# Kernel tuning notes

Hardware: AMD Instinct MI355X
Metric: run time of the kernel (lower is better)

## Reference

```python
import jax, jax.numpy as jnp
import numpy as np

L = 5          # num_layer
D = 300        # emb_dim
N = 100000     # nodes
E = 250000     # edges
G = 4000       # graphs
EPS = 1e-5


def setup_inputs() -> dict:
    key = jax.random.key(0)
    ks = jax.random.split(key, 32)
    f = lambda k, shape, s=0.02: (jax.random.normal(k, shape, dtype=jnp.float32) * s)
    inp = {
        "x_atom": jax.random.randint(ks[0], (N,), 0, 120),
        "x_chir": jax.random.randint(ks[1], (N,), 0, 3),
        "src": jax.random.randint(ks[2], (E,), 0, N),
        "dst": jax.random.randint(ks[3], (E,), 0, N),
        "edge_type": jax.random.randint(ks[4], (E,), 0, 6),
        "edge_dir": jax.random.randint(ks[5], (E,), 0, 3),
        "batch": jnp.sort(jax.random.randint(ks[6], (N,), 0, G)),
        # node feature embeddings
        "x_emb1": f(ks[7], (120, D), 0.1),
        "x_emb2": f(ks[8], (3, D), 0.1),
        # per-layer GIN params (stacked over L)
        "edge_e1": f(ks[9], (L, 6, D), 0.1),
        "edge_e2": f(ks[10], (L, 3, D), 0.1),
        "mlp_w1": f(ks[11], (L, D, 2 * D)),
        "mlp_b1": jnp.zeros((L, 2 * D), jnp.float32),
        "mlp_w2": f(ks[12], (L, 2 * D, D)),
        "mlp_b2": jnp.zeros((L, D), jnp.float32),
        # BatchNorm (inference mode: running stats)
        "bn_gamma": jnp.ones((L, D), jnp.float32),
        "bn_beta": jnp.zeros((L, D), jnp.float32),
        "bn_mean": f(ks[13], (L, D), 0.1),
        "bn_var": jax.random.uniform(ks[14], (L, D), jnp.float32, 0.5, 1.5),
        # virtual node (embedding initialized to zero in the original)
        "vn_emb": jnp.zeros((D,), jnp.float32),
        # vn MLPs: Linear -> LayerNorm -> ReLU -> Linear, L-1 of them
        "vn_w1": f(ks[15], (L - 1, D, D)),
        "vn_b1": jnp.zeros((L - 1, D), jnp.float32),
        "vn_ln_g": jnp.ones((L - 1, D), jnp.float32),
        "vn_ln_b": jnp.zeros((L - 1, D), jnp.float32),
        "vn_w2": f(ks[16], (L - 1, D, D)),
        "vn_b2": jnp.zeros((L - 1, D), jnp.float32),
    }
    return inp


def _forward(x_atom, x_chir, src, dst, edge_type, edge_dir, batch,
             x_emb1, x_emb2, edge_e1, edge_e2, mlp_w1, mlp_b1, mlp_w2, mlp_b2,
             bn_gamma, bn_beta, bn_mean, bn_var,
             vn_emb, vn_w1, vn_b1, vn_ln_g, vn_ln_b, vn_w2, vn_b2):
    n = x_atom.shape[0]
    # node counts per graph for mean pooling (guard empty graphs)
    counts = jnp.maximum(
        jax.ops.segment_sum(jnp.ones((n, 1), jnp.float32), batch, num_segments=G), 1.0)

    h = x_emb1[x_atom] + x_emb2[x_chir]                      # [N, D]
    vn_h = jnp.broadcast_to(vn_emb, (G, D))                  # [G, D]
    h = h + vn_h[batch]

    for l in range(L):
        # --- GIN conv: message = h[src] + edge_emb, scatter-add to dst ---
        edge_emb = edge_e1[l][edge_type] + edge_e2[l][edge_dir]   # [E, D]
        msg = h[src] + edge_emb
        aggr = jax.ops.segment_sum(msg, dst, num_segments=n)      # [N, D]
        # self loops: x_j = h[i], self-loop attr = (type 4, dir 0)
        aggr = aggr + h + (edge_e1[l][4] + edge_e2[l][0])
        # MLP: Linear(D,2D) -> ReLU -> Linear(2D,D)
        z = jax.nn.relu(aggr @ mlp_w1[l] + mlp_b1[l]) @ mlp_w2[l] + mlp_b2[l]
        # BatchNorm1d (eval): running stats
        z = (z - bn_mean[l]) * (bn_gamma[l] * jax.lax.rsqrt(bn_var[l] + EPS)) + bn_beta[l]
        if l < L - 1:
            z = jax.nn.relu(z)  # (dropout is identity at inference)
            # --- virtual node update ---
            pooled = jax.ops.segment_sum(z, batch, num_segments=G) / counts
            vn_new = pooled + vn_h                                # [G, D]
            t = vn_new @ vn_w1[l] + vn_b1[l]
            mu = jnp.mean(t, axis=-1, keepdims=True)
            var = jnp.var(t, axis=-1, keepdims=True)
            t = (t - mu) * jax.lax.rsqrt(var + EPS) * vn_ln_g[l] + vn_ln_b[l]
            vn_h = jax.nn.relu(t) @ vn_w2[l] + vn_b2[l]
            z = z + vn_h[batch]
        h = z
    return h


def reference(x_atom, x_chir, src, dst, edge_type, edge_dir, batch,
              x_emb1, x_emb2, edge_e1, edge_e2, mlp_w1, mlp_b1, mlp_w2, mlp_b2,
              bn_gamma, bn_beta, bn_mean, bn_var,
              vn_emb, vn_w1, vn_b1, vn_ln_g, vn_ln_b, vn_w2, vn_b2):
    return _forward(x_atom, x_chir, src, dst, edge_type, edge_dir, batch,
                    x_emb1, x_emb2, edge_e1, edge_e2, mlp_w1, mlp_b1, mlp_w2, mlp_b2,
                    bn_gamma, bn_beta, bn_mean, bn_var,
                    vn_emb, vn_w1, vn_b1, vn_ln_g, vn_ln_b, vn_w2, vn_b2)
```

## Files before the change

kernel.cpp:

```cpp
#include <hip/hip_runtime.h>

#define DD   300
#define DD2  600
#define GG   4000
#define LL   5
#define BN_EPS 1e-5f

typedef float f32x4  __attribute__((ext_vector_type(4)));
typedef short bf16x8 __attribute__((ext_vector_type(8)));

__device__ __forceinline__ unsigned short f2bf(float f) {
    unsigned int x = __float_as_uint(f);
    unsigned int r = (x + 0x7FFFu + ((x >> 16) & 1u)) >> 16;
    return (unsigned short)r;
}

__global__ __launch_bounds__(256) void k_hist(const int* __restrict__ idx, int* __restrict__ cnt, int n) {
    int i = blockIdx.x * 256 + threadIdx.x;
    if (i < n) atomicAdd(&cnt[idx[i]], 1);
}

__global__ __launch_bounds__(256) void k_scan1(const int* __restrict__ in, int* __restrict__ bsum, int n) {
    int t = threadIdx.x;
    int i = blockIdx.x * 256 + t;
    int v = (i < n) ? in[i] : 0;
    for (int off = 32; off >= 1; off >>= 1) v += __shfl_down(v, off, 64);
    __shared__ int s[4];
    if ((t & 63) == 0) s[t >> 6] = v;
    __syncthreads();
    if (t == 0) bsum[blockIdx.x] = s[0] + s[1] + s[2] + s[3];
}
__global__ __launch_bounds__(1024) void k_scan2(int* __restrict__ bsum, int nb) {
    __shared__ int s[1024];
    int t = threadIdx.x;
    int v = (t < nb) ? bsum[t] : 0;
    s[t] = v;
    __syncthreads();
    for (int off = 1; off < 1024; off <<= 1) {
        int u = (t >= off) ? s[t - off] : 0;
        __syncthreads();
        s[t] += u;
        __syncthreads();
    }
    if (t < nb) bsum[t] = s[t] - v;
}
__global__ __launch_bounds__(256) void k_scan3(const int* __restrict__ in, const int* __restrict__ boff,
                                               int* __restrict__ out, int n, int total) {
    __shared__ int s[256];
    int t = threadIdx.x;
    int i = blockIdx.x * 256 + t;
    int v = (i < n) ? in[i] : 0;
    s[t] = v;
    __syncthreads();
    for (int off = 1; off < 256; off <<= 1) {
        int u = (t >= off) ? s[t - off] : 0;
        __syncthreads();
        s[t] += u;
        __syncthreads();
    }
    if (i < n) out[i] = boff[blockIdx.x] + s[t] - v;
    if (i == 0) out[n] = total;
}

__global__ __launch_bounds__(256) void k_place(const int* __restrict__ src, const int* __restrict__ dst,
                                               const int* __restrict__ ety, const int* __restrict__ edir,
                                               const int* __restrict__ rowptr, int* __restrict__ cursor,
                                               int* __restrict__ einfo, int E) {
    int e = blockIdx.x * 256 + threadIdx.x;
    if (e >= E) return;
    int d = dst[e];
    int pos = rowptr[d] + atomicAdd(&cursor[d], 1);
    einfo[pos] = src[e] | ((ety[e] * 3 + edir[e]) << 20);
}

__global__ __launch_bounds__(256) void k_comb(const float* __restrict__ e1, const float* __restrict__ e2,
                                              float* __restrict__ comb) {
    int c = blockIdx.x, l = blockIdx.y;
    const float* r1 = e1 + ((size_t)l * 6 + (c / 3)) * DD;
    const float* r2 = e2 + ((size_t)l * 3 + (c % 3)) * DD;
    float* out = comb + ((size_t)l * 18 + c) * DD;
    for (int d = threadIdx.x; d < DD; d += 256) out[d] = r1[d] + r2[d];
}

__global__ __launch_bounds__(256) void k_init_h(const int* __restrict__ xa, const int* __restrict__ xc,
                                                const float* __restrict__ emb1, const float* __restrict__ emb2,
                                                const float* __restrict__ vne,
                                                float* __restrict__ h, int N) {
    int n = blockIdx.x;
    if (n >= N) return;
    int a = xa[n], c = xc[n];
    for (int d = threadIdx.x; d < DD; d += 256)
        h[(size_t)n * DD + d] = emb1[(size_t)a * DD + d] + emb2[(size_t)c * DD + d] + vne[d];
}

__global__ __launch_bounds__(256) void k_init_vn(const float* __restrict__ vne, float* __restrict__ vnh) {
    int g = blockIdx.x;
    for (int d = threadIdx.x; d < DD; d += 256) vnh[(size_t)g * DD + d] = vne[d];
}

__global__ __launch_bounds__(256) void k_aggr(const float* __restrict__ h,
                                              const int* __restrict__ rowptr, const int* __restrict__ einfo,
                                              const float* __restrict__ comb,
                                              const int* __restrict__ batch, const float* __restrict__ vnh,
                                              int use_vn,
                                              unsigned short* __restrict__ aggrb, int N, int Npad) {
    const int node = blockIdx.x * 4 + (threadIdx.x >> 6);
    const int lane = threadIdx.x & 63;
    if (node >= Npad) return;
    unsigned short* out = aggrb + (size_t)node * 320;
    if (node >= N) {
#pragma unroll
        for (int j = 0; j < 5; j++) out[lane + 64 * j] = 0;
        return;
    }
    float acc[5];
    const float* sc = comb + 12 * DD;
    const int p0 = rowptr[node], p1 = rowptr[node + 1];
    if (use_vn) {
        {
            const float* hs = h + (size_t)node * DD;
            const float* vs = vnh + (size_t)batch[node] * DD;
#pragma unroll
            for (int j = 0; j < 5; j++) {
                int d = lane + 64 * j;
                acc[j] = (d < DD) ? hs[d] + sc[d] + vs[d] : 0.f;
            }
        }
        for (int p = p0; p < p1; p++) {
            int info = einfo[p];
            int s = info & 0xFFFFF;
            const float* hr = h + (size_t)s * DD;
            const float* cr = comb + (size_t)(info >> 20) * DD;
            const float* vr = vnh + (size_t)batch[s] * DD;
#pragma unroll
            for (int j = 0; j < 5; j++) {
                int d = lane + 64 * j;
                if (d < DD) acc[j] += hr[d] + cr[d] + vr[d];
            }
        }
    } else {
        {
            const float* hs = h + (size_t)node * DD;
#pragma unroll
            for (int j = 0; j < 5; j++) {
                int d = lane + 64 * j;
                acc[j] = (d < DD) ? hs[d] + sc[d] : 0.f;
            }
        }
        for (int p = p0; p < p1; p++) {
            int info = einfo[p];
            const float* hr = h + (size_t)(info & 0xFFFFF) * DD;
            const float* cr = comb + (size_t)(info >> 20) * DD;
#pragma unroll
            for (int j = 0; j < 5; j++) {
                int d = lane + 64 * j;
                if (d < DD) acc[j] += hr[d] + cr[d];
            }
        }
    }
#pragma unroll
    for (int j = 0; j < 5; j++) {
        int d = lane + 64 * j;
        out[d] = (d < DD) ? f2bf(acc[j]) : (unsigned short)0;
    }
}

__global__ __launch_bounds__(256) void k_convw(const float* __restrict__ w, short* __restrict__ wt,
                                               int K, int Nn, int KP, int NP) {
    int n = blockIdx.x;
    int l = blockIdx.y;
    const float* wl = w + (size_t)l * K * Nn;
    short* wtl = wt + (size_t)l * NP * KP;
    for (int k = threadIdx.x; k < KP; k += 256) {
        float v = (k < K && n < Nn) ? wl[(size_t)k * Nn + n] : 0.f;
        wtl[(size_t)n * KP + k] = (short)f2bf(v);
    }
}

__global__ __launch_bounds__(256) void k_padb(const float* __restrict__ b, float* __restrict__ bp) {
    int l = blockIdx.y;
    int n = blockIdx.x * 256 + threadIdx.x;
    if (n < 640) bp[(size_t)l * 640 + n] = (n < DD2) ? b[(size_t)l * DD2 + n] : 0.f;
}

__global__ __launch_bounds__(256) void k_gemm1(const unsigned short* __restrict__ aggrb,
                                               const short* __restrict__ w1t,
                                               const float* __restrict__ b1p,
                                               unsigned short* __restrict__ hidden) {
    __shared__ short sA[2][64][40];
    __shared__ short sB[2][160][40];
    const int t  = threadIdx.x;
    const int m0 = blockIdx.x * 64;
    const int n0 = blockIdx.y * 160;
    const int ar = t >> 2, aq = (t & 3) << 3;

    {
        *(float4*)&sA[0][ar][aq] = *(const float4*)(aggrb + (size_t)(m0 + ar) * 320 + aq);
#pragma unroll
        for (int i = 0; i < 3; i++) {
            int c = t + (i << 8);
            if (c < 640) {
                int br = c >> 2, bq = (c & 3) << 3;
                *(float4*)&sB[0][br][bq] = *(const float4*)(w1t + (size_t)(n0 + br) * 320 + bq);
            }
        }
    }
    __syncthreads();

    const int lane = t & 63;
    const int w    = t >> 6;
    const int mrow = (w << 4) + (lane & 15);
    const int kb   = (lane >> 4) << 3;
    const int col  = lane & 15;
    const int rq   = (lane >> 4) << 2;

    f32x4 acc[10];
#pragma unroll
    for (int nt = 0; nt < 10; nt++) acc[nt] = (f32x4){0.f, 0.f, 0.f, 0.f};

    for (int ks = 0; ks < 10; ks++) {
        const int nb = ks & 1;
        const bool have = (ks + 1) < 10;
        float4 avr, bv0, bv1, bv2;
        if (have) {
            const int k0 = (ks + 1) << 5;
            avr = *(const float4*)(aggrb + (size_t)(m0 + ar) * 320 + k0 + aq);
            int c = t;
            bv0 = *(const float4*)(w1t + (size_t)(n0 + (c >> 2)) * 320 + k0 + ((c & 3) << 3));
            c = t + 256;
            bv1 = *(const float4*)(w1t + (size_t)(n0 + (c >> 2)) * 320 + k0 + ((c & 3) << 3));
            if (t < 128) {
                c = t + 512;
                bv2 = *(const float4*)(w1t + (size_t)(n0 + (c >> 2)) * 320 + k0 + ((c & 3) << 3));
            }
        }
        bf16x8 a = *(const bf16x8*)&sA[nb][mrow][kb];
#pragma unroll
        for (int nt = 0; nt < 10; nt++) {
            bf16x8 b = *(const bf16x8*)&sB[nb][(nt << 4) + col][kb];
            acc[nt] = __builtin_amdgcn_mfma_f32_16x16x32_bf16(a, b, acc[nt], 0, 0, 0);
        }
        if (have) {
            *(float4*)&sA[nb ^ 1][ar][aq] = avr;
            int c = t;
            *(float4*)&sB[nb ^ 1][c >> 2][(c & 3) << 3] = bv0;
            c = t + 256;
            *(float4*)&sB[nb ^ 1][c >> 2][(c & 3) << 3] = bv1;
            if (t < 128) {
                c = t + 512;
                *(float4*)&sB[nb ^ 1][c >> 2][(c & 3) << 3] = bv2;
            }
        }
        __syncthreads();
    }

#pragma unroll
    for (int nt = 0; nt < 10; nt++) {
        int n = n0 + (nt << 4) + col;
        float bias = b1p[n];
        int mbase = m0 + (w << 4) + rq;
#pragma unroll
        for (int r = 0; r < 4; r++) {
            float vz = fmaxf(acc[nt][r] + bias, 0.f);
            hidden[(size_t)(mbase + r) * 640 + n] = f2bf(vz);
        }
    }
}

__global__ __launch_bounds__(256) void k_gemm2(const unsigned short* __restrict__ hidden,
                                               const short* __restrict__ w2t,
                                               const float* __restrict__ b2,
                                               const float* __restrict__ bng, const float* __restrict__ bnb,
                                               const float* __restrict__ bnm, const float* __restrict__ bnv,
                                               float* __restrict__ h, int N, int relu_out) {
    __shared__ short sA[2][64][40];
    __shared__ short sB[2][160][40];
    const int t  = threadIdx.x;
    const int m0 = blockIdx.x * 64;
    const int n0 = blockIdx.y * 160;
    const int ar = t >> 2, aq = (t & 3) << 3;

    {
        *(float4*)&sA[0][ar][aq] = *(const float4*)(hidden + (size_t)(m0 + ar) * 640 + aq);
#pragma unroll
        for (int i = 0; i < 3; i++) {
            int c = t + (i << 8);
            if (c < 640) {
                int br = c >> 2, bq = (c & 3) << 3;
                *(float4*)&sB[0][br][bq] = *(const float4*)(w2t + (size_t)(n0 + br) * 640 + bq);
            }
        }
    }
    __syncthreads();

    const int lane = t & 63;
    const int w    = t >> 6;
    const int mrow = (w << 4) + (lane & 15);
    const int kb   = (lane >> 4) << 3;
    const int col  = lane & 15;
    const int rq   = (lane >> 4) << 2;

    f32x4 acc[10];
#pragma unroll
    for (int nt = 0; nt < 10; nt++) acc[nt] = (f32x4){0.f, 0.f, 0.f, 0.f};

    for (int ks = 0; ks < 20; ks++) {
        const int nb = ks & 1;
        const bool have = (ks + 1) < 20;
        float4 avr, bv0, bv1, bv2;
        if (have) {
            const int k0 = (ks + 1) << 5;
            avr = *(const float4*)(hidden + (size_t)(m0 + ar) * 640 + k0 + aq);
            int c = t;
            bv0 = *(const float4*)(w2t + (size_t)(n0 + (c >> 2)) * 640 + k0 + ((c & 3) << 3));
            c = t + 256;
            bv1 = *(const float4*)(w2t + (size_t)(n0 + (c >> 2)) * 640 + k0 + ((c & 3) << 3));
            if (t < 128) {
                c = t + 512;
                bv2 = *(const float4*)(w2t + (size_t)(n0 + (c >> 2)) * 640 + k0 + ((c & 3) << 3));
            }
        }
        bf16x8 a = *(const bf16x8*)&sA[nb][mrow][kb];
#pragma unroll
        for (int nt = 0; nt < 10; nt++) {
            bf16x8 b = *(const bf16x8*)&sB[nb][(nt << 4) + col][kb];
            acc[nt] = __builtin_amdgcn_mfma_f32_16x16x32_bf16(a, b, acc[nt], 0, 0, 0);
        }
        if (have) {
            *(float4*)&sA[nb ^ 1][ar][aq] = avr;
            int c = t;
            *(float4*)&sB[nb ^ 1][c >> 2][(c & 3) << 3] = bv0;
            c = t + 256;
            *(float4*)&sB[nb ^ 1][c >> 2][(c & 3) << 3] = bv1;
            if (t < 128) {
                c = t + 512;
                *(float4*)&sB[nb ^ 1][c >> 2][(c & 3) << 3] = bv2;
            }
        }
        __syncthreads();
    }

#pragma unroll
    for (int nt = 0; nt < 10; nt++) {
        int n = n0 + (nt << 4) + col;
        bool nok = (n < DD);
        float bz = 0.f, sc = 1.f, mB = 0.f, bB = 0.f;
        if (nok) {
            bz = b2[n];
            sc = bng[n] * rsqrtf(bnv[n] + BN_EPS);
            mB = bnm[n];
            bB = bnb[n];
        }
        int mbase = m0 + (w << 4) + rq;
#pragma unroll
        for (int r = 0; r < 4; r++) {
            int m = mbase + r;
            if (nok && m < N) {
                float z = (acc[nt][r] + bz - mB) * sc + bB;
                if (relu_out) z = fmaxf(z, 0.f);
                h[(size_t)m * DD + n] = z;
            }
        }
    }
}

__global__ __launch_bounds__(256) void k_vnpool(const float* __restrict__ h, const int* __restrict__ gptr,
                                                float* __restrict__ vnh,
                                                const float* __restrict__ w1, const float* __restrict__ b1,
                                                const float* __restrict__ lng, const float* __restrict__ lnb,
                                                const float* __restrict__ w2, const float* __restrict__ b2) {
    __shared__ float sV[DD];
    __shared__ float sT[DD];
    __shared__ float rs[4], rq[4];
    __shared__ float s_mu, s_rstd;
    int g = blockIdx.x, t = threadIdx.x;
    const int gs = gptr[g], ge = gptr[g + 1];
    const float inv = 1.0f / fmaxf((float)(ge - gs), 1.0f);

    const int j0 = t, j1 = t + 256;
    const bool g1 = (j1 < DD);

    float a0 = 0.f, a1 = 0.f;
    for (int n = gs; n < ge; n++) {
        a0 += h[(size_t)n * DD + j0];
        if (g1) a1 += h[(size_t)n * DD + j1];
    }
    sV[j0] = a0 * inv + vnh[(size_t)g * DD + j0];
    if (g1) sV[j1] = a1 * inv + vnh[(size_t)g * DD + j1];
    __syncthreads();

    a0 = 0.f; a1 = 0.f;
    for (int k = 0; k < DD; k++) {
        float v = sV[k];
        const float* wr = w1 + (size_t)k * DD;
        a0 = fmaf(v, wr[j0], a0);
        a1 = fmaf(v, g1 ? wr[j1] : 0.f, a1);
    }
    float t0 = a0 + b1[j0];
    float t1 = g1 ? (a1 + b1[j1]) : 0.f;
    sT[j0] = t0;
    if (g1) sT[j1] = t1;
    __syncthreads();

    float ps = 0.f, pq = 0.f;
    for (int i = t; i < DD; i += 256) { float x = sT[i]; ps += x; pq += x * x; }
    for (int off = 32; off >= 1; off >>= 1) { ps += __shfl_down(ps, off, 64); pq += __shfl_down(pq, off, 64); }
    int wid = t >> 6, lane = t & 63;
    if (lane == 0) { rs[wid] = ps; rq[wid] = pq; }
    __syncthreads();
    if (t == 0) {
        float S = rs[0] + rs[1] + rs[2] + rs[3];
        float Q = rq[0] + rq[1] + rq[2] + rq[3];
        float mu = S / DD;
        float var = Q / DD - mu * mu;
        s_mu = mu;
        s_rstd = rsqrtf(var + BN_EPS);
    }
    __syncthreads();
    float mu = s_mu, rstd = s_rstd;
    float r0 = fmaxf((t0 - mu) * rstd * lng[j0] + lnb[j0], 0.f);
    float r1 = g1 ? fmaxf((t1 - mu) * rstd * lng[j1] + lnb[j1], 0.f) : 0.f;
    sT[j0] = r0;
    if (g1) sT[j1] = r1;
    __syncthreads();

    float o0 = 0.f, o1 = 0.f;
    for (int k = 0; k < DD; k++) {
        float v = sT[k];
        const float* wr = w2 + (size_t)k * DD;
        o0 = fmaf(v, wr[j0], o0);
        o1 = fmaf(v, g1 ? wr[j1] : 0.f, o1);
    }
    vnh[(size_t)g * DD + j0] = o0 + b2[j0];
    if (g1) vnh[(size_t)g * DD + j1] = o1 + b2[j1];
}

extern "C" void kernel_launch(void* const* d_in, const int* in_sizes, int n_in,
                              void* d_out, int out_size, void* d_ws, size_t ws_size,
                              hipStream_t stream) {
    const int*   x_atom = (const int*)d_in[0];
    const int*   x_chir = (const int*)d_in[1];
    const int*   src    = (const int*)d_in[2];
    const int*   dst    = (const int*)d_in[3];
    const int*   ety    = (const int*)d_in[4];
    const int*   edir   = (const int*)d_in[5];
    const int*   batch  = (const int*)d_in[6];
    const float* emb1   = (const float*)d_in[7];
    const float* emb2   = (const float*)d_in[8];
    const float* e1     = (const float*)d_in[9];
    const float* e2     = (const float*)d_in[10];
    const float* w1     = (const float*)d_in[11];
    const float* b1     = (const float*)d_in[12];
    const float* w2     = (const float*)d_in[13];
    const float* b2     = (const float*)d_in[14];
    const float* bng    = (const float*)d_in[15];
    const float* bnb    = (const float*)d_in[16];
    const float* bnm    = (const float*)d_in[17];
    const float* bnv    = (const float*)d_in[18];
    const float* vne    = (const float*)d_in[19];
    const float* vw1    = (const float*)d_in[20];
    const float* vb1    = (const float*)d_in[21];
    const float* lng    = (const float*)d_in[22];
    const float* lnb    = (const float*)d_in[23];
    const float* vw2    = (const float*)d_in[24];
    const float* vb2    = (const float*)d_in[25];

    const int N = in_sizes[0];
    const int E = in_sizes[2];
    const int gx = (N + 63) / 64;
    const int Npad = gx * 64;
    const int nbN = (N + 255) / 256;
    const int nbG = (GG + 255) / 256;

    float* h = (float*)d_out;

    unsigned short* aggrb  = (unsigned short*)d_ws;
    unsigned short* hidden = aggrb + (size_t)Npad * 320;
    short*          w1t    = (short*)(hidden + (size_t)Npad * 640);
    short*          w2t    = w1t + (size_t)LL * 640 * 320;
    float*          b1p    = (float*)(w2t + (size_t)LL * 320 * 640);
    float*          comb   = b1p + (size_t)LL * 640;
    float*          vnh    = comb + (size_t)LL * 18 * DD;
    int*            deg    = (int*)(vnh + (size_t)GG * DD);
    int*            cursor = deg + N;
    int*            gcnt   = cursor + N;
    int*            rowptr = gcnt + GG;
    int*            gptr   = rowptr + (N + 1);
    int*            bsumN  = gptr + (GG + 1);
    int*            bsumG  = bsumN + 1024;
    int*            einfo  = bsumG + 1024;

    k_convw<<<dim3(640, LL), 256, 0, stream>>>(w1, w1t, DD, DD2, 320, 640);
    k_convw<<<dim3(320, LL), 256, 0, stream>>>(w2, w2t, DD2, DD, 640, 320);
    k_padb<<<dim3(3, LL), 256, 0, stream>>>(b1, b1p);
    k_comb<<<dim3(18, LL), 256, 0, stream>>>(e1, e2, comb);

    hipMemsetAsync(deg, 0, (size_t)(2 * N + GG) * sizeof(int), stream);
    k_hist<<<(E + 255) / 256, 256, 0, stream>>>(dst, deg, E);
    k_hist<<<(N + 255) / 256, 256, 0, stream>>>(batch, gcnt, N);
    k_scan1<<<nbN, 256, 0, stream>>>(deg, bsumN, N);
    k_scan2<<<1, 1024, 0, stream>>>(bsumN, nbN);
    k_scan3<<<nbN, 256, 0, stream>>>(deg, bsumN, rowptr, N, E);
    k_scan1<<<nbG, 256, 0, stream>>>(gcnt, bsumG, GG);
    k_scan2<<<1, 1024, 0, stream>>>(bsumG, nbG);
    k_scan3<<<nbG, 256, 0, stream>>>(gcnt, bsumG, gptr, GG, N);
    k_place<<<(E + 255) / 256, 256, 0, stream>>>(src, dst, ety, edir, rowptr, cursor, einfo, E);

    k_init_h<<<N, 256, 0, stream>>>(x_atom, x_chir, emb1, emb2, vne, h, N);
    k_init_vn<<<GG, 256, 0, stream>>>(vne, vnh);

    for (int l = 0; l < LL; l++) {
        k_aggr<<<Npad / 4, 256, 0, stream>>>(h, rowptr, einfo, comb + (size_t)l * 18 * DD,
                                             batch, vnh, (l > 0) ? 1 : 0, aggrb, N, Npad);
        k_gemm1<<<dim3(gx, 4), 256, 0, stream>>>(aggrb, w1t + (size_t)l * 640 * 320,
                                                 b1p + (size_t)l * 640, hidden);
        k_gemm2<<<dim3(gx, 2), 256, 0, stream>>>(hidden, w2t + (size_t)l * 320 * 640,
                                                 b2 + (size_t)l * DD,
                                                 bng + (size_t)l * DD, bnb + (size_t)l * DD,
                                                 bnm + (size_t)l * DD, bnv + (size_t)l * DD,
                                                 h, N, (l < LL - 1) ? 1 : 0);
        if (l < LL - 1) {
            k_vnpool<<<GG, 256, 0, stream>>>(h, gptr, vnh,
                                             vw1 + (size_t)l * DD * DD, vb1 + (size_t)l * DD,
                                             lng + (size_t)l * DD, lnb + (size_t)l * DD,
                                             vw2 + (size_t)l * DD * DD, vb2 + (size_t)l * DD);
        }
    }
}
```

Measured before the change: 2.497 ms.

## Split virtual-node update into pool, MFMA GEMMs and LayerNorm kernels

The per-graph virtual-node kernel ran two 300x300 matrix-vector products with scalar FMAs, rereading both weight matrices from global memory for each of the 4000 graphs. The update is now split into four kernels: a pooling kernel that writes bf16 inputs, a bf16 MFMA GEMM over all graphs with transposed, padded weights, a LayerNorm+ReLU kernel, and a second MFMA GEMM. This adds launches, an fp32 intermediate buffer and bf16 rounding of the vn activations and weights, which may affect precision.

```diff
diff --git a/kernel.cpp b/kernel.cpp
--- a/kernel.cpp
+++ b/kernel.cpp
@@ -3,6 +3,7 @@
 #define DD   300
 #define DD2  600
 #define GG   4000
+#define GPAD 4096
 #define LL   5
 #define BN_EPS 1e-5f
 
@@ -364,46 +365,123 @@
     }
 }
 
-__global__ __launch_bounds__(256) void k_vnpool(const float* __restrict__ h, const int* __restrict__ gptr,
-                                                float* __restrict__ vnh,
-                                                const float* __restrict__ w1, const float* __restrict__ b1,
-                                                const float* __restrict__ lng, const float* __restrict__ lnb,
-                                                const float* __restrict__ w2, const float* __restrict__ b2) {
-    __shared__ float sV[DD];
-    __shared__ float sT[DD];
-    __shared__ float rs[4], rq[4];
-    __shared__ float s_mu, s_rstd;
+__global__ __launch_bounds__(256) void k_pool2(const float* __restrict__ h, const int* __restrict__ gptr,
+                                               const float* __restrict__ vnh,
+                                               unsigned short* __restrict__ vnin) {
     int g = blockIdx.x, t = threadIdx.x;
     const int gs = gptr[g], ge = gptr[g + 1];
     const float inv = 1.0f / fmaxf((float)(ge - gs), 1.0f);
-
     const int j0 = t, j1 = t + 256;
     const bool g1 = (j1 < DD);
-
     float a0 = 0.f, a1 = 0.f;
     for (int n = gs; n < ge; n++) {
         a0 += h[(size_t)n * DD + j0];
         if (g1) a1 += h[(size_t)n * DD + j1];
     }
-    sV[j0] = a0 * inv + vnh[(size_t)g * DD + j0];
-    if (g1) sV[j1] = a1 * inv + vnh[(size_t)g * DD + j1];
-    __syncthreads();
-
-    a0 = 0.f; a1 = 0.f;
-    for (int k = 0; k < DD; k++) {
-        float v = sV[k];
-        const float* wr = w1 + (size_t)k * DD;
-        a0 = fmaf(v, wr[j0], a0);
-        a1 = fmaf(v, g1 ? wr[j1] : 0.f, a1);
-    }
-    float t0 = a0 + b1[j0];
-    float t1 = g1 ? (a1 + b1[j1]) : 0.f;
-    sT[j0] = t0;
-    if (g1) sT[j1] = t1;
-    __syncthreads();
-
-    float ps = 0.f, pq = 0.f;
-    for (int i = t; i < DD; i += 256) { float x = sT[i]; ps += x; pq += x * x; }
+    vnin[(size_t)g * 320 + j0] = f2bf(a0 * inv + vnh[(size_t)g * DD + j0]);
+    if (j1 < 320)
+        vnin[(size_t)g * 320 + j1] = g1 ? f2bf(a1 * inv + vnh[(size_t)g * DD + j1]) : (unsigned short)0;
+}
+
+__global__ __launch_bounds__(256) void k_vng(const unsigned short* __restrict__ A,
+                                             const short* __restrict__ Wt,
+                                             const float* __restrict__ bias,
+                                             float* __restrict__ outf,
+                                             int M) {
+    __shared__ short sA[2][64][40];
+    __shared__ short sB[2][160][40];
+    const int t  = threadIdx.x;
+    const int m0 = blockIdx.x * 64;
+    const int n0 = blockIdx.y * 160;
+    const int ar = t >> 2, aq = (t & 3) << 3;
+
+    {
+        *(float4*)&sA[0][ar][aq] = *(const float4*)(A + (size_t)(m0 + ar) * 320 + aq);
+#pragma unroll
+        for (int i = 0; i < 3; i++) {
+            int c = t + (i << 8);
+            if (c < 640) {
+                int br = c >> 2, bq = (c & 3) << 3;
+                *(float4*)&sB[0][br][bq] = *(const float4*)(Wt + (size_t)(n0 + br) * 320 + bq);
+            }
+        }
+    }
+    __syncthreads();
+
+    const int lane = t & 63;
+    const int w    = t >> 6;
+    const int mrow = (w << 4) + (lane & 15);
+    const int kb   = (lane >> 4) << 3;
+    const int col  = lane & 15;
+    const int rq   = (lane >> 4) << 2;
+
+    f32x4 acc[10];
+#pragma unroll
+    for (int nt = 0; nt < 10; nt++) acc[nt] = (f32x4){0.f, 0.f, 0.f, 0.f};
+
+    for (int ks = 0; ks < 10; ks++) {
+        const int nb = ks & 1;
+        const bool have = (ks + 1) < 10;
+        float4 avr, bv0, bv1, bv2;
+        if (have) {
+            const int k0 = (ks + 1) << 5;
+            avr = *(const float4*)(A + (size_t)(m0 + ar) * 320 + k0 + aq);
+            int c = t;
+            bv0 = *(const float4*)(Wt + (size_t)(n0 + (c >> 2)) * 320 + k0 + ((c & 3) << 3));
+            c = t + 256;
+            bv1 = *(const float4*)(Wt + (size_t)(n0 + (c >> 2)) * 320 + k0 + ((c & 3) << 3));
+            if (t < 128) {
+                c = t + 512;
+                bv2 = *(const float4*)(Wt + (size_t)(n0 + (c >> 2)) * 320 + k0 + ((c & 3) << 3));
+            }
+        }
+        bf16x8 a = *(const bf16x8*)&sA[nb][mrow][kb];
+#pragma unroll
+        for (int nt = 0; nt < 10; nt++) {
+            bf16x8 b = *(const bf16x8*)&sB[nb][(nt << 4) + col][kb];
+            acc[nt] = __builtin_amdgcn_mfma_f32_16x16x32_bf16(a, b, acc[nt], 0, 0, 0);
+        }
+        if (have) {
+            *(float4*)&sA[nb ^ 1][ar][aq] = avr;
+            int c = t;
+            *(float4*)&sB[nb ^ 1][c >> 2][(c & 3) << 3] = bv0;
+            c = t + 256;
+            *(float4*)&sB[nb ^ 1][c >> 2][(c & 3) << 3] = bv1;
+            if (t < 128) {
+                c = t + 512;
+                *(float4*)&sB[nb ^ 1][c >> 2][(c & 3) << 3] = bv2;
+            }
+        }
+        __syncthreads();
+    }
+
+#pragma unroll
+    for (int nt = 0; nt < 10; nt++) {
+        int n = n0 + (nt << 4) + col;
+        bool nok = (n < DD);
+        float bz = nok ? bias[n] : 0.f;
+        int mbase = m0 + (w << 4) + rq;
+#pragma unroll
+        for (int r = 0; r < 4; r++) {
+            int m = mbase + r;
+            if (nok && m < M)
+                outf[(size_t)m * DD + n] = acc[nt][r] + bz;
+        }
+    }
+}
+
+__global__ __launch_bounds__(256) void k_ln(const float* __restrict__ tbuf,
+                                            const float* __restrict__ lng, const float* __restrict__ lnb,
+                                            unsigned short* __restrict__ vnrelu) {
+    __shared__ float rs[4], rq[4];
+    __shared__ float s_mu, s_rstd;
+    int g = blockIdx.x, t = threadIdx.x;
+    const int j0 = t, j1 = t + 256;
+    const bool g1 = (j1 < DD);
+    float t0 = tbuf[(size_t)g * DD + j0];
+    float t1 = g1 ? tbuf[(size_t)g * DD + j1] : 0.f;
+    float ps = t0 + t1;
+    float pq = t0 * t0 + t1 * t1;
     for (int off = 32; off >= 1; off >>= 1) { ps += __shfl_down(ps, off, 64); pq += __shfl_down(pq, off, 64); }
     int wid = t >> 6, lane = t & 63;
     if (lane == 0) { rs[wid] = ps; rq[wid] = pq; }
@@ -419,20 +497,11 @@
     __syncthreads();
     float mu = s_mu, rstd = s_rstd;
     float r0 = fmaxf((t0 - mu) * rstd * lng[j0] + lnb[j0], 0.f);
-    float r1 = g1 ? fmaxf((t1 - mu) * rstd * lng[j1] + lnb[j1], 0.f) : 0.f;
-    sT[j0] = r0;
-    if (g1) sT[j1] = r1;
-    __syncthreads();
-
-    float o0 = 0.f, o1 = 0.f;
-    for (int k = 0; k < DD; k++) {
-        float v = sT[k];
-        const float* wr = w2 + (size_t)k * DD;
-        o0 = fmaf(v, wr[j0], o0);
-        o1 = fmaf(v, g1 ? wr[j1] : 0.f, o1);
-    }
-    vnh[(size_t)g * DD + j0] = o0 + b2[j0];
-    if (g1) vnh[(size_t)g * DD + j1] = o1 + b2[j1];
+    vnrelu[(size_t)g * 320 + j0] = f2bf(r0);
+    if (j1 < 320) {
+        float r1 = g1 ? fmaxf((t1 - mu) * rstd * lng[j1] + lnb[j1], 0.f) : 0.f;
+        vnrelu[(size_t)g * 320 + j1] = g1 ? f2bf(r1) : (unsigned short)0;
+    }
 }
 
 extern "C" void kernel_launch(void* const* d_in, const int* in_sizes, int n_in,
@@ -478,9 +547,14 @@
     unsigned short* hidden = aggrb + (size_t)Npad * 320;
     short*          w1t    = (short*)(hidden + (size_t)Npad * 640);
     short*          w2t    = w1t + (size_t)LL * 640 * 320;
-    float*          b1p    = (float*)(w2t + (size_t)LL * 320 * 640);
+    short*          vw1t   = w2t + (size_t)LL * 320 * 640;
+    short*          vw2t   = vw1t + (size_t)(LL - 1) * 320 * 320;
+    unsigned short* vnin   = (unsigned short*)(vw2t + (size_t)(LL - 1) * 320 * 320);
+    unsigned short* vnrelu = vnin + (size_t)GPAD * 320;
+    float*          b1p    = (float*)(vnrelu + (size_t)GPAD * 320);
     float*          comb   = b1p + (size_t)LL * 640;
-    float*          vnh    = comb + (size_t)LL * 18 * DD;
+    float*          tbuf   = comb + (size_t)LL * 18 * DD;
+    float*          vnh    = tbuf + (size_t)GG * DD;
     int*            deg    = (int*)(vnh + (size_t)GG * DD);
     int*            cursor = deg + N;
     int*            gcnt   = cursor + N;
@@ -492,6 +566,8 @@
 
     k_convw<<<dim3(640, LL), 256, 0, stream>>>(w1, w1t, DD, DD2, 320, 640);
     k_convw<<<dim3(320, LL), 256, 0, stream>>>(w2, w2t, DD2, DD, 640, 320);
+    k_convw<<<dim3(320, LL - 1), 256, 0, stream>>>(vw1, vw1t, DD, DD, 320, 320);
+    k_convw<<<dim3(320, LL - 1), 256, 0, stream>>>(vw2, vw2t, DD, DD, 320, 320);
     k_padb<<<dim3(3, LL), 256, 0, stream>>>(b1, b1p);
     k_comb<<<dim3(18, LL), 256, 0, stream>>>(e1, e2, comb);
 
@@ -520,10 +596,12 @@
                                                  bnm + (size_t)l * DD, bnv + (size_t)l * DD,
                                                  h, N, (l < LL - 1) ? 1 : 0);
         if (l < LL - 1) {
-            k_vnpool<<<GG, 256, 0, stream>>>(h, gptr, vnh,
-                                             vw1 + (size_t)l * DD * DD, vb1 + (size_t)l * DD,
-                                             lng + (size_t)l * DD, lnb + (size_t)l * DD,
-                                             vw2 + (size_t)l * DD * DD, vb2 + (size_t)l * DD);
-        }
-    }
-}
+            k_pool2<<<GG, 256, 0, stream>>>(h, gptr, vnh, vnin);
+            k_vng<<<dim3(GPAD / 64, 2), 256, 0, stream>>>(vnin, vw1t + (size_t)l * 320 * 320,
+                                                          vb1 + (size_t)l * DD, tbuf, GG);
+            k_ln<<<GG, 256, 0, stream>>>(tbuf, lng + (size_t)l * DD, lnb + (size_t)l * DD, vnrelu);
+            k_vng<<<dim3(GPAD / 64, 2), 256, 0, stream>>>(vnrelu, vw2t + (size_t)l * 320 * 320,
+                                                          vb2 + (size_t)l * DD, vnh, GG);
+        }
+    }
+}
```

After: 2.181 ms. 1.14x faster.
